# Performance work log

Hardware: AMD Instinct MI355X
Metric: run time of the kernel (lower is better)

Reference implementation:

```python
import jax, jax.numpy as jnp
import numpy as np

N = 4096            # num nodes
D = 256             # feature dim
NUM_SUPER_NODES = 6
THRESHOLD = 0.0
EPS = 1e-10
DENSITY = 0.02      # pre-symmetrization edge density


def setup_inputs() -> dict:
    key = jax.random.key(0)
    kx, ka = jax.random.split(key)
    X = jax.random.normal(kx, (N, D), dtype=jnp.float32)
    U = jax.random.uniform(ka, (N, N), dtype=jnp.float32)
    A = (U < DENSITY).astype(jnp.float32)
    A = jnp.maximum(A, A.T)                      # symmetric 0/1 adjacency
    A = A * (1.0 - jnp.eye(N, dtype=jnp.float32))  # no self-loops
    return {"X": X, "A": A}


def _greedy_labels(sim_np, n, num_super, threshold):
    """Sequential greedy union-find merge over pairs sorted by similarity.
    Matches torch: stable descending sort on sim only; merge until
    n - merged <= num_super; relabel roots in first-occurrence order.
    Inherently sequential/data-dependent -> done in numpy on concrete values
    (the torch original also detaches via .item())."""
    iu, ju = np.triu_indices(n, k=1)
    sims = sim_np[iu, ju]
    keep = sims >= threshold
    iu, ju, sims = iu[keep], ju[keep], sims[keep]
    order = np.argsort(-sims, kind="stable")     # stable desc == list.sort(reverse=True)
    parent = np.arange(n)

    def find(i):
        while parent[i] != i:
            parent[i] = parent[parent[i]]        # path halving
            i = parent[i]
        return i

    merged = 0
    for k in order:
        pi, pj = find(int(iu[k])), find(int(ju[k]))
        if pi != pj:
            parent[pj] = pi
            merged += 1
            if n - merged <= num_super:
                break
    mapping = {}
    labels = np.empty(n, dtype=np.int64)
    nl = 0
    for i in range(n):
        r = find(i)
        if r not in mapping:
            mapping[r] = nl
            nl += 1
        labels[i] = mapping[r]
    return labels, nl


def _build_P(A):
    """Vectorized pairwise Jaccard (replaces O(n^2) python loop) + greedy merge."""
    n = A.shape[0]
    A_bin = (A > 0).astype(jnp.float32)
    deg = A_bin.sum(axis=1)                      # |N(i)|
    inter = A_bin @ A_bin.T                      # [n,n] pairwise |Ni & Nj|
    union = deg[:, None] + deg[None, :] - inter  # |Ni | Nj|
    sim = jnp.where(union > 0, inter / jnp.maximum(union, 1.0), 0.0)
    labels, m = _greedy_labels(np.asarray(sim), n, NUM_SUPER_NODES, THRESHOLD)
    P_prime = jax.nn.one_hot(jnp.asarray(labels), m, dtype=jnp.float32)  # [n, m]
    sizes = P_prime.sum(axis=0)
    return P_prime / jnp.sqrt(sizes + EPS)[None, :]   # P = P' @ diag(1/sqrt(sizes+eps))


def reference(X, A):
    P = _build_P(A)                               # [n, m], m == NUM_SUPER_NODES
    X_coarse = P.T @ X                            # [m, D]
    A_coarse = P.T @ A @ P                        # [m, m]
    return (X_coarse, A_coarse, P)
```

## Files before the change

kernel.cpp:

```cpp
#include <hip/hip_runtime.h>

typedef unsigned long long u64;
typedef unsigned short u16;
typedef unsigned char u8;

#define NN 4096
#define NCH 64
#define NSUP 6

__global__ __launch_bounds__(256) void k_packdeg(const float* __restrict__ A,
                                                 u64* __restrict__ bits,
                                                 u16* __restrict__ deg,
                                                 float* out, int out_n,
                                                 int* comp, int* ncomp, int* mstcnt) {
  int t = threadIdx.x;
  int w = t >> 6, lane = t & 63;
  int row = blockIdx.x * 4 + w;
  const float* rp = A + (size_t)row * NN;
  u64 my = 0;
  int dsum = 0;
#pragma unroll 8
  for (int k = 0; k < 64; ++k) {
    float v = rp[k * 64 + lane];
    u64 m = __ballot(v > 0.0f);
    dsum += __popcll(m);
    if (lane == k) my = m;
  }
  bits[(size_t)row * NCH + lane] = my;
  if (lane == 0) deg[row] = (u16)dsum;
  int g = blockIdx.x * 256 + t;
  if (g < out_n) out[g] = 0.0f;
  if (g < NN) comp[g] = g;
  if (g == 0) { *ncomp = NN; *mstcnt = 0; }
}

__global__ __launch_bounds__(256) void k_inter(const u64* __restrict__ bits,
                                               u8* __restrict__ inter) {
  __shared__ ulonglong2 L[2][64 * 16];
  int b = blockIdx.x;
  int by = (int)((129.0f - sqrtf(16641.0f - 8.0f * (float)b)) * 0.5f) - 1;
  if (by < 0) by = 0;
#define CUM(y) (64 * (y) - ((y) * ((y) - 1)) / 2)
  while (by < 63 && CUM(by + 1) <= b) ++by;
  while (CUM(by) > b) --by;
  int bx = by + (b - CUM(by));
#undef CUM
  int i0 = by * 64, j0 = bx * 64;
  int t = threadIdx.x;
  int tx = t & 15, ty = t >> 4;
  int rowA[4], swA[4], rowB[4], swB[4];
#pragma unroll
  for (int a = 0; a < 4; ++a) {
    rowA[a] = ty * 4 + a; swA[a] = (rowA[a] ^ (rowA[a] >> 2)) & 7;
    rowB[a] = tx * 4 + a; swB[a] = (rowB[a] ^ (rowB[a] >> 2)) & 7;
  }
  int cuL = t & 15, rg = t >> 4;
  int acc[4][4] = {};
  for (int st = 0; st < 2; ++st) {
    __syncthreads();
#pragma unroll
    for (int rr = 0; rr < 4; ++rr) {
      int row = rg * 4 + rr;
      int sw = (row ^ (row >> 2)) & 7;
      L[0][row * 16 + (cuL ^ sw)] =
          reinterpret_cast<const ulonglong2*>(bits + (size_t)(i0 + row) * NCH)[st * 16 + cuL];
      L[1][row * 16 + (cuL ^ sw)] =
          reinterpret_cast<const ulonglong2*>(bits + (size_t)(j0 + row) * NCH)[st * 16 + cuL];
    }
    __syncthreads();
    for (int cu = 0; cu < 16; ++cu) {
      ulonglong2 av[4], bv[4];
#pragma unroll
      for (int a = 0; a < 4; ++a) av[a] = L[0][rowA[a] * 16 + (cu ^ swA[a])];
#pragma unroll
      for (int b2 = 0; b2 < 4; ++b2) bv[b2] = L[1][rowB[b2] * 16 + (cu ^ swB[b2])];
#pragma unroll
      for (int a = 0; a < 4; ++a)
#pragma unroll
        for (int b2 = 0; b2 < 4; ++b2)
          acc[a][b2] += __popcll(av[a].x & bv[b2].x) + __popcll(av[a].y & bv[b2].y);
    }
  }
#pragma unroll
  for (int a = 0; a < 4; ++a) {
    int i = i0 + ty * 4 + a;
    uchar4 wv;
    wv.x = (u8)acc[a][0]; wv.y = (u8)acc[a][1];
    wv.z = (u8)acc[a][2]; wv.w = (u8)acc[a][3];
    *reinterpret_cast<uchar4*>(inter + (size_t)i * NN + j0 + tx * 4) = wv;
  }
  if (bx != by) {
#pragma unroll
    for (int b2 = 0; b2 < 4; ++b2) {
      int j = j0 + tx * 4 + b2;
      uchar4 wv;
      wv.x = (u8)acc[0][b2]; wv.y = (u8)acc[1][b2];
      wv.z = (u8)acc[2][b2]; wv.w = (u8)acc[3][b2];
      *reinterpret_cast<uchar4*>(inter + (size_t)j * NN + i0 + ty * 4) = wv;
    }
  }
}

__global__ __launch_bounds__(256) void k_scan(const u8* __restrict__ inter,
                                              const u16* __restrict__ deg,
                                              const int* __restrict__ comp,
                                              const int* __restrict__ ncomp,
                                              u64* __restrict__ nkey,
                                              int* __restrict__ nu) {
  if (*ncomp <= 1) return;
  __shared__ u16 comp_s[NN];
  __shared__ u16 deg_s[NN];
  int t = threadIdx.x;
  for (int i = t; i < NN / 8; i += 256) {
    int4 ca = reinterpret_cast<const int4*>(comp)[i * 2];
    int4 cb = reinterpret_cast<const int4*>(comp)[i * 2 + 1];
    uint4 pk;
    pk.x = (unsigned)ca.x | ((unsigned)ca.y << 16);
    pk.y = (unsigned)ca.z | ((unsigned)ca.w << 16);
    pk.z = (unsigned)cb.x | ((unsigned)cb.y << 16);
    pk.w = (unsigned)cb.z | ((unsigned)cb.w << 16);
    reinterpret_cast<uint4*>(comp_s)[i] = pk;
    reinterpret_cast<uint4*>(deg_s)[i] = reinterpret_cast<const uint4*>(deg)[i];
  }
  __syncthreads();
  int w = t >> 6, lane = t & 63;
  int v = blockIdx.x * 4 + w;
  int cv = (int)comp_s[v];
  int dv = (int)deg_s[v];
  const u8* row = inter + (size_t)v * NN;
  u64 key = 0;
  for (int it = 0; it < 4; ++it) {
    int ub = it * 1024 + lane * 16;
    uint4 pv = *reinterpret_cast<const uint4*>(row + ub);
    uint4 dg0 = reinterpret_cast<const uint4*>(deg_s)[ub >> 3];
    uint4 dg1 = reinterpret_cast<const uint4*>(deg_s)[(ub >> 3) + 1];
    uint4 cs0 = reinterpret_cast<const uint4*>(comp_s)[ub >> 3];
    uint4 cs1 = reinterpret_cast<const uint4*>(comp_s)[(ub >> 3) + 1];
    unsigned pw[4] = { pv.x, pv.y, pv.z, pv.w };
    unsigned dw[8] = { dg0.x, dg0.y, dg0.z, dg0.w, dg1.x, dg1.y, dg1.z, dg1.w };
    unsigned cw[8] = { cs0.x, cs0.y, cs0.z, cs0.w, cs1.x, cs1.y, cs1.z, cs1.w };
#pragma unroll
    for (int k = 0; k < 16; ++k) {
      int iv = (int)((pw[k >> 2] >> ((k & 3) * 8)) & 0xFF);
      int du = (int)((dw[k >> 1] >> ((k & 1) * 16)) & 0xFFFF);
      int cu = (int)((cw[k >> 1] >> ((k & 1) * 16)) & 0xFFFF);
      int un = dv + du - iv;
      float s = (un > 0) ? ((float)iv / (float)un) : 0.0f;
      unsigned sb = __float_as_uint(s);
      u64 kk = (cu != cv)
                   ? (((u64)sb << 32) | (u64)(0xFFFFFFFFu - (unsigned)(ub + k)))
                   : 0ull;
      if (kk > key) key = kk;
    }
  }
#pragma unroll
  for (int off = 32; off > 0; off >>= 1) {
    unsigned lo = (unsigned)key, hi = (unsigned)(key >> 32);
    unsigned olo = __shfl_xor(lo, off, 64), ohi = __shfl_xor(hi, off, 64);
    u64 o = ((u64)ohi << 32) | (u64)olo;
    if (o > key) key = o;
  }
  if (lane == 0) {
    u64 pk = 0; int u = -1;
    if (key != 0ull) {
      unsigned simb = (unsigned)(key >> 32);
      u = (int)(0xFFFFFFFFu - (unsigned)(key & 0xFFFFFFFFull));
      int i = v < u ? v : u, j = v < u ? u : v;
      unsigned idx = (unsigned)i * (unsigned)(2 * NN - i - 1) / 2u + (unsigned)(j - i - 1);
      pk = ((u64)simb << 24) | (u64)(0xFFFFFFu - idx);
    }
    nkey[v] = pk; nu[v] = u;
  }
}

__global__ __launch_bounds__(1024) void k_merge(const u64* __restrict__ nkey,
                                                const int* __restrict__ nu,
                                                int* comp, int* ncomp, int* mstcnt,
                                                u64* mkey, int* mi, int* mj,
                                                int* labels_g, float* invs_g, float* out) {
  if (*ncomp <= 1) return;
  __shared__ int parent_s[NN];
  __shared__ u64 cbest_s[NN];
  __shared__ unsigned char mk_s[NN];
  __shared__ int roots[16];
  __shared__ int rcnt, cnt_s, chg_s, changed;
  __shared__ int szs[8];
  __shared__ float ivs[8];
  int t = threadIdx.x;
  for (int c = t; c < NN; c += 1024) { parent_s[c] = c; cbest_s[c] = 0ull; }
  __syncthreads();
  for (int v = t; v < NN; v += 1024) {
    u64 k = nkey[v];
    if (k) atomicMax(&cbest_s[comp[v]], k);
  }
  __syncthreads();
  for (int v = t; v < NN; v += 1024) {
    u64 k = nkey[v];
    if (!k) continue;
    int c = comp[v];
    if (k == cbest_s[c]) {
      int u = nu[v];
      int cu = comp[u];
      bool mutual = (cbest_s[cu] == k);
      if (!mutual || v < u) {
        int slot = atomicAdd(mstcnt, 1);
        if (slot < 4352) { mkey[slot] = k; mi[slot] = v; mj[slot] = u; }
      }
      parent_s[c] = cu;
    }
  }
  __syncthreads();
  for (int c = t; c < NN; c += 1024) {
    int pc = parent_s[c];
    if (parent_s[pc] == c && c < pc) parent_s[c] = c;
  }
  __syncthreads();
  for (int it = 0; it < 13; ++it) {
    if (t == 0) chg_s = 0;
    __syncthreads();
    for (int c = t; c < NN; c += 1024) {
      int p1 = parent_s[c], p2 = parent_s[p1];
      if (p1 != p2) { parent_s[c] = p2; chg_s = 1; }
    }
    __syncthreads();
    if (!chg_s) break;
  }
  for (int c = t; c < NN; c += 1024) mk_s[c] = 0;
  if (t == 0) cnt_s = 0;
  __syncthreads();
  for (int v = t; v < NN; v += 1024) {
    int nc = parent_s[comp[v]];
    comp[v] = nc;
    mk_s[nc] = 1;
  }
  __syncthreads();
  int lc = 0;
  for (int c = t; c < NN; c += 1024) lc += mk_s[c];
  atomicAdd(&cnt_s, lc);
  __syncthreads();
  if (t == 0) *ncomp = cnt_s;
  __syncthreads();
  if (cnt_s != 1) return;
  int* rr = reinterpret_cast<int*>(cbest_s);
  u64* rk = cbest_s + 2048;
  int* rs = reinterpret_cast<int*>(cbest_s + 3072);
  int nm = *mstcnt;
  if (nm < 0) nm = 0;
  if (nm > 4352) nm = 4352;
  for (int v = t; v < NN; v += 1024) parent_s[v] = v;
  for (int pass = 0; pass < NSUP - 1; ++pass) {
    u64 bk = ~0ull; int bsel = -1;
    for (int e = t; e < nm; e += 1024) { u64 k = mkey[e]; if (k < bk) { bk = k; bsel = e; } }
    rk[t] = bk; rs[t] = bsel;
    __syncthreads();
    for (int s = 512; s > 0; s >>= 1) {
      if (t < s && rk[t + s] < rk[t]) { rk[t] = rk[t + s]; rs[t] = rs[t + s]; }
      __syncthreads();
    }
    if (t == 0 && rs[0] >= 0) mkey[rs[0]] = ~0ull;
    __syncthreads();
  }
  for (int round = 0; round < 64; ++round) {
    if (t == 0) changed = 0;
    __syncthreads();
    for (int e = t; e < nm; e += 1024) {
      if (mkey[e] == ~0ull) continue;
      int a = parent_s[mi[e]], b = parent_s[mj[e]];
      if (a == b) continue;
      int m = a < b ? a : b, M = a < b ? b : a;
      int old = atomicMin(&parent_s[M], m);
      if (old > m) changed = 1;
    }
    __syncthreads();
    for (int rep = 0; rep < 3; ++rep) {
      for (int v = t; v < NN; v += 1024) parent_s[v] = parent_s[parent_s[v]];
      __syncthreads();
    }
    int ch = changed;
    __syncthreads();
    if (!ch) break;
  }
  for (int rep = 0; rep < 13; ++rep) {
    for (int v = t; v < NN; v += 1024) parent_s[v] = parent_s[parent_s[v]];
    __syncthreads();
  }
  if (t == 0) rcnt = 0;
  __syncthreads();
  for (int v = t; v < NN; v += 1024)
    if (parent_s[v] == v) { int s = atomicAdd(&rcnt, 1); if (s < 16) roots[s] = v; }
  __syncthreads();
  if (t == 0) {
    int c = rcnt > 16 ? 16 : rcnt;
    for (int a = 1; a < c; ++a) {
      int x = roots[a]; int b2 = a - 1;
      while (b2 >= 0 && roots[b2] > x) { roots[b2 + 1] = roots[b2]; --b2; }
      roots[b2 + 1] = x;
    }
  }
  if (t < 8) szs[t] = 0;
  __syncthreads();
  if (t < rcnt && t < 16) rr[roots[t]] = t;
  __syncthreads();
  for (int v = t; v < NN; v += 1024) {
    int lab = rr[parent_s[v]];
    labels_g[v] = lab;
    atomicAdd(&szs[lab], 1);
  }
  __syncthreads();
  if (t < rcnt && t < 8) {
    float iv = 1.0f / sqrtf((float)szs[t] + 1e-10f);
    ivs[t] = iv; invs_g[t] = iv;
  }
  __syncthreads();
  for (int v = t; v < NN; v += 1024) {
    int lab = rr[parent_s[v]];
    float* base = out + 1572 + v * 6;
#pragma unroll
    for (int b2 = 0; b2 < 6; ++b2) base[b2] = (b2 == lab) ? ivs[lab] : 0.0f;
  }
}

__global__ __launch_bounds__(256) void k_coarse(const float* __restrict__ X,
                                                const u64* __restrict__ bits,
                                                const int* __restrict__ labels,
                                                const float* __restrict__ invs,
                                                float* out) {
  int t = threadIdx.x;
  if (blockIdx.x < 64) {
    __shared__ float acc[6][256];
    __shared__ int labs[64];
    __shared__ float ivl[64];
#pragma unroll
    for (int m = 0; m < 6; ++m) acc[m][t] = 0.0f;
    if (t < 64) { int v = blockIdx.x * 64 + t; int l = labels[v]; labs[t] = l; ivl[t] = invs[l]; }
    __syncthreads();
    int v0 = blockIdx.x * 64;
    for (int r = 0; r < 64; ++r) {
      float x = X[(size_t)(v0 + r) * 256 + t];
      acc[labs[r]][t] += ivl[r] * x;
    }
    __syncthreads();
#pragma unroll
    for (int m = 0; m < 6; ++m) atomicAdd(&out[m * 256 + t], acc[m][t]);
  } else {
    __shared__ unsigned char labs8[NN];
    __shared__ float accA[36];
    __shared__ float ivsl[8];
    for (int v = t; v < NN; v += 256) labs8[v] = (unsigned char)labels[v];
    if (t < 36) accA[t] = 0.0f;
    if (t < 6) ivsl[t] = invs[t];
    __syncthreads();
    int i = (blockIdx.x - 64) * 256 + t;
    u64 cnt = 0;
    const u64* row = bits + (size_t)i * NCH;
    for (int c = 0; c < NCH; ++c) {
      u64 wm = row[c];
      while (wm) {
        int j = (c << 6) + __builtin_ctzll(wm);
        wm &= wm - 1;
        cnt += 1ull << (labs8[j] * 10);
      }
    }
    int li = labs8[i];
    float fi = ivsl[li];
#pragma unroll
    for (int b = 0; b < 6; ++b) {
      float cb = (float)((cnt >> (b * 10)) & 1023ull);
      if (cb != 0.0f) atomicAdd(&accA[li * 6 + b], fi * ivsl[b] * cb);
    }
    __syncthreads();
    if (t < 36) atomicAdd(&out[1536 + t], accA[t]);
  }
}

extern "C" void kernel_launch(void* const* d_in, const int* in_sizes, int n_in,
                              void* d_out, int out_size, void* d_ws, size_t ws_size,
                              hipStream_t stream) {
  const float* X = (const float*)d_in[0];
  const float* A = (const float*)d_in[1];
  float* out = (float*)d_out;

  char* wp = (char*)d_ws;
  size_t off = 0;
#define WALLOC(ty, name, count) \
  ty* name = (ty*)(wp + off);   \
  off += (((size_t)(count) * sizeof(ty)) + 255) & ~(size_t)255;
  WALLOC(u64, bits, (size_t)NN * NCH)
  WALLOC(u8, inter, (size_t)NN * NN)
  WALLOC(u16, deg, NN)
  WALLOC(int, comp, NN)
  WALLOC(u64, nkey, NN)
  WALLOC(int, nu, NN)
  WALLOC(u64, mkey, 4352)
  WALLOC(int, mi, 4352)
  WALLOC(int, mj, 4352)
  WALLOC(int, labels, NN)
  WALLOC(float, invs, 8)
  WALLOC(int, ncomp, 1)
  WALLOC(int, mstcnt, 1)
#undef WALLOC
  if (off > ws_size) return;

  k_packdeg<<<NN / 4, 256, 0, stream>>>(A, bits, deg, out, out_size, comp, ncomp, mstcnt);
  k_inter<<<2080, 256, 0, stream>>>(bits, inter);
  for (int ph = 0; ph < 12; ++ph) {
    k_scan<<<NN / 4, 256, 0, stream>>>(inter, deg, comp, ncomp, nkey, nu);
    k_merge<<<1, 1024, 0, stream>>>(nkey, nu, comp, ncomp, mstcnt, mkey, mi, mj,
                                    labels, invs, out);
  }
  k_coarse<<<80, 256, 0, stream>>>(X, bits, labels, invs, out);
}
```

Before: 365.9 us.

## Fuse per-phase merge into scan kernel with redundant per-block merge

Replaces the separate single-block merge kernel with a merge step recomputed redundantly by every block at the start of the next scan phase, using ping-pong neighbor-key buffers. This roughly halves the number of kernel launches and removes the serialized 1024-thread merge launch between scans. Shared state is compacted to 16-bit arrays. In exchange every block repeats the merge work, and block 0 writes comp and ncomp while other blocks may still be reading them, which risks races.

```diff
diff --git a/kernel.cpp b/kernel.cpp
--- a/kernel.cpp
+++ b/kernel.cpp
@@ -7,6 +7,7 @@
 #define NN 4096
 #define NCH 64
 #define NSUP 6
+#define NPB 1024
 
 __global__ __launch_bounds__(256) void k_packdeg(const float* __restrict__ A,
                                                  u64* __restrict__ bits,
@@ -101,15 +102,21 @@
   }
 }
 
-__global__ __launch_bounds__(256) void k_scan(const u8* __restrict__ inter,
-                                              const u16* __restrict__ deg,
-                                              const int* __restrict__ comp,
-                                              const int* __restrict__ ncomp,
-                                              u64* __restrict__ nkey,
-                                              int* __restrict__ nu) {
+__global__ __launch_bounds__(256) void k_phase(
+    const u8* __restrict__ inter, const u16* __restrict__ deg,
+    int* comp, int* ncomp, int* mstcnt,
+    const u64* __restrict__ nkeyR, const int* __restrict__ nuR,
+    u64* __restrict__ nkeyW, int* __restrict__ nuW,
+    u64* mkey, int* mi, int* mj, int ph, int doScan,
+    int* labels_g, float* invs_g, float* out) {
   if (*ncomp <= 1) return;
-  __shared__ u16 comp_s[NN];
-  __shared__ u16 deg_s[NN];
+  __shared__ u64 big[NN];
+  __shared__ u16 a16[NN];
+  __shared__ u16 b16[NN];
+  __shared__ int roots[16];
+  __shared__ int rcnt, cnt_s, chg_s, changed;
+  __shared__ int szs[8];
+  __shared__ float ivs[8];
   int t = threadIdx.x;
   for (int i = t; i < NN / 8; i += 256) {
     int4 ca = reinterpret_cast<const int4*>(comp)[i * 2];
@@ -119,13 +126,162 @@
     pk.y = (unsigned)ca.z | ((unsigned)ca.w << 16);
     pk.z = (unsigned)cb.x | ((unsigned)cb.y << 16);
     pk.w = (unsigned)cb.z | ((unsigned)cb.w << 16);
-    reinterpret_cast<uint4*>(comp_s)[i] = pk;
+    reinterpret_cast<uint4*>(a16)[i] = pk;
+  }
+  if (ph > 0) {
+    for (int c = t; c < NN; c += 256) { big[c] = 0ull; b16[c] = (u16)c; }
+    __syncthreads();
+    for (int v = t; v < NN; v += 256) {
+      u64 k = nkeyR[v];
+      if (k) atomicMax(&big[(int)a16[v]], k);
+    }
+    __syncthreads();
+    for (int v = t; v < NN; v += 256) {
+      u64 k = nkeyR[v];
+      if (!k) continue;
+      int c = (int)a16[v];
+      if (k == big[c]) {
+        int u = nuR[v];
+        int cu = (int)a16[u];
+        bool mutual = (big[cu] == k);
+        if (blockIdx.x == 0 && (!mutual || v < u)) {
+          int slot = atomicAdd(mstcnt, 1);
+          if (slot < 4352) { mkey[slot] = k; mi[slot] = v; mj[slot] = u; }
+        }
+        b16[c] = (u16)cu;
+      }
+    }
+    __syncthreads();
+    for (int c = t; c < NN; c += 256) {
+      int pc = (int)b16[c];
+      if ((int)b16[pc] == c && c < pc) b16[c] = (u16)c;
+    }
+    __syncthreads();
+    for (int it = 0; it < 13; ++it) {
+      if (t == 0) chg_s = 0;
+      __syncthreads();
+      for (int c = t; c < NN; c += 256) {
+        int p1 = (int)b16[c], p2 = (int)b16[p1];
+        if (p1 != p2) { b16[c] = (u16)p2; chg_s = 1; }
+      }
+      __syncthreads();
+      if (!chg_s) break;
+    }
+    for (int v = t; v < NN; v += 256) a16[v] = b16[(int)a16[v]];
+    __syncthreads();
+    u64* mark = big;
+    if (t < 64) mark[t] = 0ull;
+    if (t == 0) cnt_s = 0;
+    __syncthreads();
+    for (int v = t; v < NN; v += 256) {
+      int nc = (int)a16[v];
+      atomicOr(&mark[nc >> 6], 1ull << (nc & 63));
+    }
+    __syncthreads();
+    if (t < 64) atomicAdd(&cnt_s, __popcll(mark[t]));
+    __syncthreads();
+    int cnt = cnt_s;
+    if (blockIdx.x == 0) {
+      for (int i = t; i < NN / 4; i += 256) {
+        int4 w4;
+        w4.x = (int)a16[i * 4];     w4.y = (int)a16[i * 4 + 1];
+        w4.z = (int)a16[i * 4 + 2]; w4.w = (int)a16[i * 4 + 3];
+        reinterpret_cast<int4*>(comp)[i] = w4;
+      }
+      if (t == 0) *ncomp = cnt;
+    }
+    if (cnt == 1) {
+      if (blockIdx.x != 0) return;
+      u16* p16 = a16;
+      u16* rr16 = b16;
+      u64* rk = big;
+      int* rs = reinterpret_cast<int*>(big + 256);
+      int nm = *mstcnt;
+      if (nm < 0) nm = 0;
+      if (nm > 4352) nm = 4352;
+      for (int v = t; v < NN; v += 256) p16[v] = (u16)v;
+      __syncthreads();
+      for (int pass = 0; pass < NSUP - 1; ++pass) {
+        u64 bk = ~0ull; int bsel = -1;
+        for (int e = t; e < nm; e += 256) { u64 k = mkey[e]; if (k < bk) { bk = k; bsel = e; } }
+        rk[t] = bk; rs[t] = bsel;
+        __syncthreads();
+        for (int s = 128; s > 0; s >>= 1) {
+          if (t < s && rk[t + s] < rk[t]) { rk[t] = rk[t + s]; rs[t] = rs[t + s]; }
+          __syncthreads();
+        }
+        if (t == 0 && rs[0] >= 0) mkey[rs[0]] = ~0ull;
+        __syncthreads();
+      }
+      for (int round = 0; round < 64; ++round) {
+        if (t == 0) changed = 0;
+        __syncthreads();
+        for (int e = t; e < nm; e += 256) {
+          if (mkey[e] == ~0ull) continue;
+          int a = (int)p16[mi[e]], b = (int)p16[mj[e]];
+          if (a == b) continue;
+          int m = a < b ? a : b, M = a < b ? b : a;
+          if ((int)p16[M] > m) { p16[M] = (u16)m; changed = 1; }
+        }
+        __syncthreads();
+        for (int rep = 0; rep < 3; ++rep) {
+          for (int v = t; v < NN; v += 256) p16[v] = p16[(int)p16[v]];
+          __syncthreads();
+        }
+        int ch = changed;
+        __syncthreads();
+        if (!ch) break;
+      }
+      for (int rep = 0; rep < 13; ++rep) {
+        for (int v = t; v < NN; v += 256) p16[v] = p16[(int)p16[v]];
+        __syncthreads();
+      }
+      if (t == 0) rcnt = 0;
+      __syncthreads();
+      for (int v = t; v < NN; v += 256)
+        if ((int)p16[v] == v) { int s = atomicAdd(&rcnt, 1); if (s < 16) roots[s] = v; }
+      __syncthreads();
+      if (t == 0) {
+        int c = rcnt > 16 ? 16 : rcnt;
+        for (int a = 1; a < c; ++a) {
+          int x = roots[a]; int b2 = a - 1;
+          while (b2 >= 0 && roots[b2] > x) { roots[b2 + 1] = roots[b2]; --b2; }
+          roots[b2 + 1] = x;
+        }
+      }
+      if (t < 8) szs[t] = 0;
+      __syncthreads();
+      if (t < rcnt && t < 16) rr16[roots[t]] = (u16)t;
+      __syncthreads();
+      for (int v = t; v < NN; v += 256) {
+        int lab = (int)rr16[(int)p16[v]];
+        labels_g[v] = lab;
+        atomicAdd(&szs[lab], 1);
+      }
+      __syncthreads();
+      if (t < rcnt && t < 8) {
+        float iv = 1.0f / sqrtf((float)szs[t] + 1e-10f);
+        ivs[t] = iv; invs_g[t] = iv;
+      }
+      __syncthreads();
+      for (int v = t; v < NN; v += 256) {
+        int lab = (int)rr16[(int)p16[v]];
+        float* base = out + 1572 + v * 6;
+#pragma unroll
+        for (int b2 = 0; b2 < 6; ++b2) base[b2] = (b2 == lab) ? ivs[lab] : 0.0f;
+      }
+      return;
+    }
+  }
+  if (!doScan) return;
+  u16* deg_s = reinterpret_cast<u16*>(big);
+  __syncthreads();
+  for (int i = t; i < NN / 8; i += 256)
     reinterpret_cast<uint4*>(deg_s)[i] = reinterpret_cast<const uint4*>(deg)[i];
-  }
   __syncthreads();
   int w = t >> 6, lane = t & 63;
   int v = blockIdx.x * 4 + w;
-  int cv = (int)comp_s[v];
+  int cv = (int)a16[v];
   int dv = (int)deg_s[v];
   const u8* row = inter + (size_t)v * NN;
   u64 key = 0;
@@ -134,8 +290,8 @@
     uint4 pv = *reinterpret_cast<const uint4*>(row + ub);
     uint4 dg0 = reinterpret_cast<const uint4*>(deg_s)[ub >> 3];
     uint4 dg1 = reinterpret_cast<const uint4*>(deg_s)[(ub >> 3) + 1];
-    uint4 cs0 = reinterpret_cast<const uint4*>(comp_s)[ub >> 3];
-    uint4 cs1 = reinterpret_cast<const uint4*>(comp_s)[(ub >> 3) + 1];
+    uint4 cs0 = reinterpret_cast<const uint4*>(a16)[ub >> 3];
+    uint4 cs1 = reinterpret_cast<const uint4*>(a16)[(ub >> 3) + 1];
     unsigned pw[4] = { pv.x, pv.y, pv.z, pv.w };
     unsigned dw[8] = { dg0.x, dg0.y, dg0.z, dg0.w, dg1.x, dg1.y, dg1.z, dg1.w };
     unsigned cw[8] = { cs0.x, cs0.y, cs0.z, cs0.w, cs1.x, cs1.y, cs1.z, cs1.w };
@@ -169,154 +325,7 @@
       unsigned idx = (unsigned)i * (unsigned)(2 * NN - i - 1) / 2u + (unsigned)(j - i - 1);
       pk = ((u64)simb << 24) | (u64)(0xFFFFFFu - idx);
     }
-    nkey[v] = pk; nu[v] = u;
-  }
-}
-
-__global__ __launch_bounds__(1024) void k_merge(const u64* __restrict__ nkey,
-                                                const int* __restrict__ nu,
-                                                int* comp, int* ncomp, int* mstcnt,
-                                                u64* mkey, int* mi, int* mj,
-                                                int* labels_g, float* invs_g, float* out) {
-  if (*ncomp <= 1) return;
-  __shared__ int parent_s[NN];
-  __shared__ u64 cbest_s[NN];
-  __shared__ unsigned char mk_s[NN];
-  __shared__ int roots[16];
-  __shared__ int rcnt, cnt_s, chg_s, changed;
-  __shared__ int szs[8];
-  __shared__ float ivs[8];
-  int t = threadIdx.x;
-  for (int c = t; c < NN; c += 1024) { parent_s[c] = c; cbest_s[c] = 0ull; }
-  __syncthreads();
-  for (int v = t; v < NN; v += 1024) {
-    u64 k = nkey[v];
-    if (k) atomicMax(&cbest_s[comp[v]], k);
-  }
-  __syncthreads();
-  for (int v = t; v < NN; v += 1024) {
-    u64 k = nkey[v];
-    if (!k) continue;
-    int c = comp[v];
-    if (k == cbest_s[c]) {
-      int u = nu[v];
-      int cu = comp[u];
-      bool mutual = (cbest_s[cu] == k);
-      if (!mutual || v < u) {
-        int slot = atomicAdd(mstcnt, 1);
-        if (slot < 4352) { mkey[slot] = k; mi[slot] = v; mj[slot] = u; }
-      }
-      parent_s[c] = cu;
-    }
-  }
-  __syncthreads();
-  for (int c = t; c < NN; c += 1024) {
-    int pc = parent_s[c];
-    if (parent_s[pc] == c && c < pc) parent_s[c] = c;
-  }
-  __syncthreads();
-  for (int it = 0; it < 13; ++it) {
-    if (t == 0) chg_s = 0;
-    __syncthreads();
-    for (int c = t; c < NN; c += 1024) {
-      int p1 = parent_s[c], p2 = parent_s[p1];
-      if (p1 != p2) { parent_s[c] = p2; chg_s = 1; }
-    }
-    __syncthreads();
-    if (!chg_s) break;
-  }
-  for (int c = t; c < NN; c += 1024) mk_s[c] = 0;
-  if (t == 0) cnt_s = 0;
-  __syncthreads();
-  for (int v = t; v < NN; v += 1024) {
-    int nc = parent_s[comp[v]];
-    comp[v] = nc;
-    mk_s[nc] = 1;
-  }
-  __syncthreads();
-  int lc = 0;
-  for (int c = t; c < NN; c += 1024) lc += mk_s[c];
-  atomicAdd(&cnt_s, lc);
-  __syncthreads();
-  if (t == 0) *ncomp = cnt_s;
-  __syncthreads();
-  if (cnt_s != 1) return;
-  int* rr = reinterpret_cast<int*>(cbest_s);
-  u64* rk = cbest_s + 2048;
-  int* rs = reinterpret_cast<int*>(cbest_s + 3072);
-  int nm = *mstcnt;
-  if (nm < 0) nm = 0;
-  if (nm > 4352) nm = 4352;
-  for (int v = t; v < NN; v += 1024) parent_s[v] = v;
-  for (int pass = 0; pass < NSUP - 1; ++pass) {
-    u64 bk = ~0ull; int bsel = -1;
-    for (int e = t; e < nm; e += 1024) { u64 k = mkey[e]; if (k < bk) { bk = k; bsel = e; } }
-    rk[t] = bk; rs[t] = bsel;
-    __syncthreads();
-    for (int s = 512; s > 0; s >>= 1) {
-      if (t < s && rk[t + s] < rk[t]) { rk[t] = rk[t + s]; rs[t] = rs[t + s]; }
-      __syncthreads();
-    }
-    if (t == 0 && rs[0] >= 0) mkey[rs[0]] = ~0ull;
-    __syncthreads();
-  }
-  for (int round = 0; round < 64; ++round) {
-    if (t == 0) changed = 0;
-    __syncthreads();
-    for (int e = t; e < nm; e += 1024) {
-      if (mkey[e] == ~0ull) continue;
-      int a = parent_s[mi[e]], b = parent_s[mj[e]];
-      if (a == b) continue;
-      int m = a < b ? a : b, M = a < b ? b : a;
-      int old = atomicMin(&parent_s[M], m);
-      if (old > m) changed = 1;
-    }
-    __syncthreads();
-    for (int rep = 0; rep < 3; ++rep) {
-      for (int v = t; v < NN; v += 1024) parent_s[v] = parent_s[parent_s[v]];
-      __syncthreads();
-    }
-    int ch = changed;
-    __syncthreads();
-    if (!ch) break;
-  }
-  for (int rep = 0; rep < 13; ++rep) {
-    for (int v = t; v < NN; v += 1024) parent_s[v] = parent_s[parent_s[v]];
-    __syncthreads();
-  }
-  if (t == 0) rcnt = 0;
-  __syncthreads();
-  for (int v = t; v < NN; v += 1024)
-    if (parent_s[v] == v) { int s = atomicAdd(&rcnt, 1); if (s < 16) roots[s] = v; }
-  __syncthreads();
-  if (t == 0) {
-    int c = rcnt > 16 ? 16 : rcnt;
-    for (int a = 1; a < c; ++a) {
-      int x = roots[a]; int b2 = a - 1;
-      while (b2 >= 0 && roots[b2] > x) { roots[b2 + 1] = roots[b2]; --b2; }
-      roots[b2 + 1] = x;
-    }
-  }
-  if (t < 8) szs[t] = 0;
-  __syncthreads();
-  if (t < rcnt && t < 16) rr[roots[t]] = t;
-  __syncthreads();
-  for (int v = t; v < NN; v += 1024) {
-    int lab = rr[parent_s[v]];
-    labels_g[v] = lab;
-    atomicAdd(&szs[lab], 1);
-  }
-  __syncthreads();
-  if (t < rcnt && t < 8) {
-    float iv = 1.0f / sqrtf((float)szs[t] + 1e-10f);
-    ivs[t] = iv; invs_g[t] = iv;
-  }
-  __syncthreads();
-  for (int v = t; v < NN; v += 1024) {
-    int lab = rr[parent_s[v]];
-    float* base = out + 1572 + v * 6;
-#pragma unroll
-    for (int b2 = 0; b2 < 6; ++b2) base[b2] = (b2 == lab) ? ivs[lab] : 0.0f;
+    nkeyW[v] = pk; nuW[v] = u;
   }
 }
 
@@ -389,8 +398,10 @@
   WALLOC(u8, inter, (size_t)NN * NN)
   WALLOC(u16, deg, NN)
   WALLOC(int, comp, NN)
-  WALLOC(u64, nkey, NN)
-  WALLOC(int, nu, NN)
+  WALLOC(u64, nkeyA, NN)
+  WALLOC(u64, nkeyB, NN)
+  WALLOC(int, nuA, NN)
+  WALLOC(int, nuB, NN)
   WALLOC(u64, mkey, 4352)
   WALLOC(int, mi, 4352)
   WALLOC(int, mj, 4352)
@@ -403,10 +414,16 @@
 
   k_packdeg<<<NN / 4, 256, 0, stream>>>(A, bits, deg, out, out_size, comp, ncomp, mstcnt);
   k_inter<<<2080, 256, 0, stream>>>(bits, inter);
-  for (int ph = 0; ph < 12; ++ph) {
-    k_scan<<<NN / 4, 256, 0, stream>>>(inter, deg, comp, ncomp, nkey, nu);
-    k_merge<<<1, 1024, 0, stream>>>(nkey, nu, comp, ncomp, mstcnt, mkey, mi, mj,
-                                    labels, invs, out);
+  for (int ph = 0; ph <= 12; ++ph) {
+    int doScan = (ph < 12) ? 1 : 0;
+    u64* nW = (ph & 1) ? nkeyB : nkeyA;
+    int* uW = (ph & 1) ? nuB : nuA;
+    const u64* nR = (ph & 1) ? nkeyA : nkeyB;
+    const int* uR = (ph & 1) ? nuA : nuB;
+    k_phase<<<doScan ? NPB : 1, 256, 0, stream>>>(inter, deg, comp, ncomp, mstcnt,
+                                                  nR, uR, nW, uW,
+                                                  mkey, mi, mj, ph, doScan,
+                                                  labels, invs, out);
   }
   k_coarse<<<80, 256, 0, stream>>>(X, bits, labels, invs, out);
 }
```

Result: slower. 602.3 us (+64.6%).

## Cache per-node top-4 neighbor keys to skip full row rescans in Boruvka phases

Applied to the files above, without the earlier changes.

Adds an initial scan kernel that computes, for each node, the top-4 similarity candidates across all other nodes and stores them. Later Boruvka phases first check these cached candidates against the current components and only rescan the full intersection row when all four fall inside the node's own component. This targets the repeated full 4096x4096 byte reads of the intersection matrix across phases. The cost is a heavier first scan with a top-4 insertion network and shuffle reductions, plus a small extra buffer. The loop is also reordered so merge runs first using the initial scan results.

```diff
diff --git a/kernel.cpp b/kernel.cpp
--- a/kernel.cpp
+++ b/kernel.cpp
@@ -7,6 +7,20 @@
 #define NN 4096
 #define NCH 64
 #define NSUP 6
+
+__device__ __forceinline__ u64 gkey(int v, int u, unsigned sb) {
+  int i = v < u ? v : u, j = v < u ? u : v;
+  unsigned idx = (unsigned)i * (unsigned)(2 * NN - i - 1) / 2u + (unsigned)(j - i - 1);
+  return ((u64)sb << 24) | (u64)(0xFFFFFFu - idx);
+}
+
+__device__ __forceinline__ void ins4(u64& a0, u64& a1, u64& a2, u64& a3, u64 kk) {
+  bool g0 = kk > a0, g1 = kk > a1, g2 = kk > a2, g3 = kk > a3;
+  a3 = g3 ? (g2 ? a2 : kk) : a3;
+  a2 = g2 ? (g1 ? a1 : kk) : a2;
+  a1 = g1 ? (g0 ? a0 : kk) : a1;
+  a0 = g0 ? kk : a0;
+}
 
 __global__ __launch_bounds__(256) void k_packdeg(const float* __restrict__ A,
                                                  u64* __restrict__ bits,
@@ -101,8 +115,64 @@
   }
 }
 
+__global__ __launch_bounds__(256) void k_scan0(const u8* __restrict__ inter,
+                                               const u16* __restrict__ deg,
+                                               u64* __restrict__ tk,
+                                               u64* __restrict__ nkey,
+                                               int* __restrict__ nu) {
+  __shared__ u16 deg_s[NN];
+  int t = threadIdx.x;
+  for (int i = t; i < NN / 8; i += 256)
+    reinterpret_cast<uint4*>(deg_s)[i] = reinterpret_cast<const uint4*>(deg)[i];
+  __syncthreads();
+  int w = t >> 6, lane = t & 63;
+  int v = blockIdx.x * 4 + w;
+  int dv = (int)deg_s[v];
+  const u8* row = inter + (size_t)v * NN;
+  u64 a0 = 0, a1 = 0, a2 = 0, a3 = 0;
+  for (int it = 0; it < 4; ++it) {
+    int ub = it * 1024 + lane * 16;
+    uint4 pv = *reinterpret_cast<const uint4*>(row + ub);
+    uint4 dg0 = reinterpret_cast<const uint4*>(deg_s)[ub >> 3];
+    uint4 dg1 = reinterpret_cast<const uint4*>(deg_s)[(ub >> 3) + 1];
+    unsigned pw[4] = { pv.x, pv.y, pv.z, pv.w };
+    unsigned dw[8] = { dg0.x, dg0.y, dg0.z, dg0.w, dg1.x, dg1.y, dg1.z, dg1.w };
+#pragma unroll
+    for (int k = 0; k < 16; ++k) {
+      int u = ub + k;
+      int iv = (int)((pw[k >> 2] >> ((k & 3) * 8)) & 0xFF);
+      int du = (int)((dw[k >> 1] >> ((k & 1) * 16)) & 0xFFFF);
+      int un = dv + du - iv;
+      float s = (un > 0) ? ((float)iv / (float)un) : 0.0f;
+      u64 kk = (u != v)
+                   ? (((u64)__float_as_uint(s) << 32) | (u64)(0xFFFFFFFFu - (unsigned)u))
+                   : 0ull;
+      ins4(a0, a1, a2, a3, kk);
+    }
+  }
+#pragma unroll
+  for (int off = 1; off < 64; off <<= 1) {
+    u64 b0 = __shfl_xor(a0, off, 64);
+    u64 b1 = __shfl_xor(a1, off, 64);
+    u64 b2 = __shfl_xor(a2, off, 64);
+    u64 b3 = __shfl_xor(a3, off, 64);
+    ins4(a0, a1, a2, a3, b0);
+    ins4(a0, a1, a2, a3, b1);
+    ins4(a0, a1, a2, a3, b2);
+    ins4(a0, a1, a2, a3, b3);
+  }
+  if (lane == 0) {
+    u64* tv = tk + (size_t)v * 4;
+    tv[0] = a0; tv[1] = a1; tv[2] = a2; tv[3] = a3;
+    int u0 = (int)(0xFFFFFFFFu - (unsigned)(a0 & 0xFFFFFFFFull));
+    nkey[v] = gkey(v, u0, (unsigned)(a0 >> 32));
+    nu[v] = u0;
+  }
+}
+
 __global__ __launch_bounds__(256) void k_scan(const u8* __restrict__ inter,
                                               const u16* __restrict__ deg,
+                                              const u64* __restrict__ tk,
                                               const int* __restrict__ comp,
                                               const int* __restrict__ ncomp,
                                               u64* __restrict__ nkey,
@@ -110,7 +180,9 @@
   if (*ncomp <= 1) return;
   __shared__ u16 comp_s[NN];
   __shared__ u16 deg_s[NN];
+  __shared__ int anyneed;
   int t = threadIdx.x;
+  if (t == 0) anyneed = 0;
   for (int i = t; i < NN / 8; i += 256) {
     int4 ca = reinterpret_cast<const int4*>(comp)[i * 2];
     int4 cb = reinterpret_cast<const int4*>(comp)[i * 2 + 1];
@@ -120,12 +192,35 @@
     pk.z = (unsigned)cb.x | ((unsigned)cb.y << 16);
     pk.w = (unsigned)cb.z | ((unsigned)cb.w << 16);
     reinterpret_cast<uint4*>(comp_s)[i] = pk;
-    reinterpret_cast<uint4*>(deg_s)[i] = reinterpret_cast<const uint4*>(deg)[i];
   }
   __syncthreads();
   int w = t >> 6, lane = t & 63;
   int v = blockIdx.x * 4 + w;
   int cv = (int)comp_s[v];
+  u64 gk = 0; int bu = -1; bool need = true;
+  const u64* tv = tk + (size_t)v * 4;
+#pragma unroll
+  for (int e = 0; e < 4; ++e) {
+    u64 cand = tv[e];
+    unsigned uu = 0xFFFFFFFFu - (unsigned)(cand & 0xFFFFFFFFull);
+    if (need && (int)comp_s[uu] != cv) {
+      need = false;
+      gk = gkey(v, (int)uu, (unsigned)(cand >> 32));
+      bu = (int)uu;
+    }
+  }
+  if (!need) {
+    if (lane == 0) { nkey[v] = gk; nu[v] = bu; }
+  } else if (lane == 0) {
+    atomicOr(&anyneed, 1 << w);
+  }
+  __syncthreads();
+  int needmask = anyneed;
+  if (!needmask) return;
+  for (int i = t; i < NN / 8; i += 256)
+    reinterpret_cast<uint4*>(deg_s)[i] = reinterpret_cast<const uint4*>(deg)[i];
+  __syncthreads();
+  if (!(needmask >> w & 1)) return;
   int dv = (int)deg_s[v];
   const u8* row = inter + (size_t)v * NN;
   u64 key = 0;
@@ -146,9 +241,8 @@
       int cu = (int)((cw[k >> 1] >> ((k & 1) * 16)) & 0xFFFF);
       int un = dv + du - iv;
       float s = (un > 0) ? ((float)iv / (float)un) : 0.0f;
-      unsigned sb = __float_as_uint(s);
       u64 kk = (cu != cv)
-                   ? (((u64)sb << 32) | (u64)(0xFFFFFFFFu - (unsigned)(ub + k)))
+                   ? (((u64)__float_as_uint(s) << 32) | (u64)(0xFFFFFFFFu - (unsigned)(ub + k)))
                    : 0ull;
       if (kk > key) key = kk;
     }
@@ -165,9 +259,7 @@
     if (key != 0ull) {
       unsigned simb = (unsigned)(key >> 32);
       u = (int)(0xFFFFFFFFu - (unsigned)(key & 0xFFFFFFFFull));
-      int i = v < u ? v : u, j = v < u ? u : v;
-      unsigned idx = (unsigned)i * (unsigned)(2 * NN - i - 1) / 2u + (unsigned)(j - i - 1);
-      pk = ((u64)simb << 24) | (u64)(0xFFFFFFu - idx);
+      pk = gkey(v, u, simb);
     }
     nkey[v] = pk; nu[v] = u;
   }
@@ -388,6 +480,7 @@
   WALLOC(u64, bits, (size_t)NN * NCH)
   WALLOC(u8, inter, (size_t)NN * NN)
   WALLOC(u16, deg, NN)
+  WALLOC(u64, tk, (size_t)NN * 4)
   WALLOC(int, comp, NN)
   WALLOC(u64, nkey, NN)
   WALLOC(int, nu, NN)
@@ -403,10 +496,12 @@
 
   k_packdeg<<<NN / 4, 256, 0, stream>>>(A, bits, deg, out, out_size, comp, ncomp, mstcnt);
   k_inter<<<2080, 256, 0, stream>>>(bits, inter);
+  k_scan0<<<NN / 4, 256, 0, stream>>>(inter, deg, tk, nkey, nu);
   for (int ph = 0; ph < 12; ++ph) {
-    k_scan<<<NN / 4, 256, 0, stream>>>(inter, deg, comp, ncomp, nkey, nu);
     k_merge<<<1, 1024, 0, stream>>>(nkey, nu, comp, ncomp, mstcnt, mkey, mi, mj,
                                     labels, invs, out);
+    if (ph < 11)
+      k_scan<<<NN / 4, 256, 0, stream>>>(inter, deg, tk, comp, ncomp, nkey, nu);
   }
   k_coarse<<<80, 256, 0, stream>>>(X, bits, labels, invs, out);
 }
```

After: 364.1 us. About the same (-0.5%).
